# Kernel tuning notes

Hardware: AMD Instinct MI355X
Metric: run time of the kernel (lower is better)

The kernel has to match this reference:

```python
import jax, jax.numpy as jnp
import numpy as np

B, S, H, DK = 8, 2048, 1024, 64


def setup_inputs() -> dict:
    key = jax.random.key(0)
    ks = jax.random.split(key, 8)
    x = jax.random.normal(ks[0], (B, S, H), dtype=jnp.float32)
    # padding at the tail: positions >= length are pad (True)
    lengths = jax.random.randint(ks[1], (B,), S // 2, S + 1)
    padding_mask = jnp.arange(S)[None, :] >= lengths[:, None]  # [B,S] bool, True = pad
    sc = 1.0 / np.sqrt(H)
    Wq = jax.random.normal(ks[2], (H, DK), dtype=jnp.float32) * sc
    Wk = jax.random.normal(ks[3], (H, DK), dtype=jnp.float32) * sc
    Wv = jax.random.normal(ks[4], (H, DK), dtype=jnp.float32) * sc
    bq = jnp.zeros((DK,), dtype=jnp.float32)
    bk = jnp.zeros((DK,), dtype=jnp.float32)
    bv = jnp.zeros((DK,), dtype=jnp.float32)
    return {"x": x, "padding_mask": padding_mask, "Wq": Wq, "bq": bq,
            "Wk": Wk, "bk": bk, "Wv": Wv, "bv": bv}


def reference(x, padding_mask, Wq, bq, Wk, bk, Wv, bv):
    # Single-head attention, dropout_pe = 0 (identity), masking=True (causal).
    d_k = Wq.shape[-1]
    Q = jnp.einsum('bsh,hd->bsd', x, Wq) + bq
    K = jnp.einsum('bsh,hd->bsd', x, Wk) + bk
    V = jnp.einsum('bsh,hd->bsd', x, Wv) + bv
    scores = jnp.einsum('bqd,bkd->bqk', Q, K) / jnp.sqrt(jnp.asarray(d_k, x.dtype))
    neg_inf = jnp.finfo(scores.dtype).min
    # padding mask over keys: [B,1,S]
    scores = jnp.where(padding_mask[:, None, :], neg_inf, scores)
    # causal mask: strictly upper triangular is disallowed
    seq = scores.shape[-1]
    causal = jnp.triu(jnp.ones((seq, seq), dtype=bool), k=1)
    scores = jnp.where(causal[None, :, :], neg_inf, scores)
    W = jax.nn.softmax(scores, axis=-1)
    # zero out attention rows for padded query positions: [B,S,1]
    W = jnp.where(padding_mask[:, :, None], 0.0, W)
    return jnp.einsum('bqk,bkd->bqd', W, V)
```

## Files before the change

kernel.cpp:

```cpp
#include <hip/hip_runtime.h>
#include <hip/hip_bf16.h>

#define NB 8
#define SEQ 2048
#define HD 1024
#define DK 64

#define QSCALE 0.1803368801111244f
#define FIXMAX2 11.541560327111708f

typedef __attribute__((ext_vector_type(4))) float f32x4;
typedef __attribute__((ext_vector_type(8))) short bf16x8;
typedef __attribute__((ext_vector_type(4))) unsigned short u16x4;

__device__ __forceinline__ short f2bf(float f) {
    union { float f; unsigned u; } v; v.f = f;
    unsigned r = v.u + 0x7fffu + ((v.u >> 16) & 1u);
    return (short)(r >> 16);
}
__device__ __forceinline__ bf16x8 pack8(f32x4 v0, f32x4 v1) {
    union { bf16x8 v; __hip_bfloat162 h[4]; } u;
    u.h[0] = __float22bfloat162_rn(make_float2(v0[0], v0[1]));
    u.h[1] = __float22bfloat162_rn(make_float2(v0[2], v0[3]));
    u.h[2] = __float22bfloat162_rn(make_float2(v1[0], v1[1]));
    u.h[3] = __float22bfloat162_rn(make_float2(v1[2], v1[3]));
    return u.v;
}

__global__ void prep_kernel(const unsigned* __restrict__ mask,
                            const float* __restrict__ Wq, const float* __restrict__ Wk,
                            const float* __restrict__ Wv,
                            int* __restrict__ lengths, short* __restrict__ Wp) {
    if (blockIdx.x < 768) {
        int idx = blockIdx.x * 256 + threadIdx.x;
        int j = idx & 7, lane = (idx >> 3) & 63;
        int slot = idx >> 9;
        int fr = slot % 3, q2 = slot / 3;
        int kh = q2 & 1, cg = (q2 >> 1) & 3, kbg = q2 >> 3;
        int g = lane >> 4, c = lane & 15;
        int n = cg * 3 + fr;
        int m = n >> 2, colm = (n & 3) * 16 + c;
        int k = kbg * 64 + kh * 32 + g * 8 + j;
        const float* W = (m == 0) ? Wq : (m == 1) ? Wk : Wv;
        Wp[idx] = f2bf(W[(size_t)k * DK + colm]);
        return;
    }
    __shared__ int sdet;
    __shared__ int scnt;
    int b = blockIdx.x - 768, t = threadIdx.x;
    if (t == 0) { sdet = 0; scnt = 0; }
    __syncthreads();
    int det = 0;
    for (int i = t; i < 4096; i += 256) {
        unsigned w = mask[i];
        if (w > 1u && w != 0x3F800000u) det = 1;
    }
    if (det) atomicOr(&sdet, 1);
    __syncthreads();
    int cnt = 0;
    if (sdet) {
        const unsigned char* m8 = (const unsigned char*)mask;
        for (int s = t; s < SEQ; s += 256) cnt += (m8[b * SEQ + s] == 0) ? 1 : 0;
    } else {
        for (int s = t; s < SEQ; s += 256) cnt += (mask[b * SEQ + s] == 0u) ? 1 : 0;
    }
    atomicAdd(&scnt, cnt);
    __syncthreads();
    if (t == 0) lengths[b] = scnt;
}

__global__ __launch_bounds__(512, 2) void qkv_kernel(
    const float* __restrict__ x,
    const float* __restrict__ bq, const float* __restrict__ bk, const float* __restrict__ bv,
    const short* __restrict__ Wp,
    short* __restrict__ Q, short* __restrict__ K, short* __restrict__ Vt) {
    __shared__ float xs[2][64][64];
    int t = threadIdx.x;
    int w = t >> 6, lane = t & 63;
    int g = lane >> 4, c = lane & 15;
    int rg = w >> 2, cg = w & 3;
    int r0 = blockIdx.x * 64;
    int bb = r0 >> 11, sbase = r0 & (SEQ - 1);

    int srow = t >> 3, sc8 = t & 7;
    const float* xsrc = x + (size_t)(r0 + srow) * HD + sc8 * 8;
    float* wbase = &xs[0][0][0];
    int wo0 = srow * 64 + (((2 * sc8) ^ (srow & 15)) << 2);
    int wo1 = srow * 64 + (((2 * sc8 + 1) ^ (srow & 15)) << 2);

    const short* wpw = Wp + (size_t)cg * 2 * 3 * 512 + (size_t)lane * 8;

    f32x4 z = {0.f, 0.f, 0.f, 0.f};
    f32x4 acc[2][3];
    #pragma unroll
    for (int rf = 0; rf < 2; rf++)
        #pragma unroll
        for (int fr = 0; fr < 3; fr++) acc[rf][fr] = z;

    {
        f32x4 x0 = *(const f32x4*)xsrc;
        f32x4 x1 = *(const f32x4*)(xsrc + 4);
        *(f32x4*)(wbase + wo0) = x0;
        *(f32x4*)(wbase + wo1) = x1;
    }
    bf16x8 Bc[2][3];
    #pragma unroll
    for (int kh = 0; kh < 2; kh++)
        #pragma unroll
        for (int fr = 0; fr < 3; fr++)
            Bc[kh][fr] = *(const bf16x8*)(wpw + kh * 1536 + fr * 512);
    __syncthreads();

    const float* rbase0 = &xs[0][0][0] + (rg * 32 + c) * 64;
    #pragma unroll
    for (int kbg = 0; kbg < 16; kbg++) {
        int cur = kbg & 1;
        f32x4 nx0, nx1;
        bf16x8 Bn[2][3];
        if (kbg < 15) {
            const float* p = xsrc + (kbg + 1) * 64;
            nx0 = *(const f32x4*)p;
            nx1 = *(const f32x4*)(p + 4);
            #pragma unroll
            for (int kh = 0; kh < 2; kh++)
                #pragma unroll
                for (int fr = 0; fr < 3; fr++)
                    Bn[kh][fr] = *(const bf16x8*)(wpw + (kbg + 1) * 12288 + kh * 1536 + fr * 512);
        }
        bf16x8 Af[2][2];
        #pragma unroll
        for (int rf = 0; rf < 2; rf++)
            #pragma unroll
            for (int kh = 0; kh < 2; kh++) {
                const float* rp = rbase0 + cur * 4096 + rf * 1024;
                int lg = kh * 8 + 2 * g;
                f32x4 lo = *(const f32x4*)(rp + ((lg ^ c) << 2));
                f32x4 hi = *(const f32x4*)(rp + (((lg + 1) ^ c) << 2));
                Af[rf][kh] = pack8(lo, hi);
            }
        #pragma unroll
        for (int kh = 0; kh < 2; kh++)
            #pragma unroll
            for (int fr = 0; fr < 3; fr++)
                #pragma unroll
                for (int rf = 0; rf < 2; rf++)
                    acc[rf][fr] = __builtin_amdgcn_mfma_f32_16x16x32_bf16(Af[rf][kh], Bc[kh][fr], acc[rf][fr], 0, 0, 0);
        if (kbg < 15) {
            float* wb = wbase + (cur ^ 1) * 4096;
            *(f32x4*)(wb + wo0) = nx0;
            *(f32x4*)(wb + wo1) = nx1;
            #pragma unroll
            for (int kh = 0; kh < 2; kh++)
                #pragma unroll
                for (int fr = 0; fr < 3; fr++) Bc[kh][fr] = Bn[kh][fr];
        }
        __syncthreads();
    }

    #pragma unroll
    for (int rf = 0; rf < 2; rf++)
        #pragma unroll
        for (int fr = 0; fr < 3; fr++) {
            int n = cg * 3 + fr;
            int m = n >> 2, colm = (n & 3) * 16 + c;
            const float* bias = (m == 0) ? bq : (m == 1) ? bk : bv;
            float bv_ = bias[colm];
            if (m == 2) {
                u16x4 pk;
                #pragma unroll
                for (int j = 0; j < 4; j++) pk[j] = (unsigned short)f2bf(acc[rf][fr][j] + bv_);
                int srw = sbase + rg * 32 + rf * 16 + 4 * g;
                *(u16x4*)(Vt + (size_t)bb * DK * SEQ + (size_t)colm * SEQ + srw) = pk;
            } else {
                #pragma unroll
                for (int j = 0; j < 4; j++) {
                    int row = r0 + rg * 32 + rf * 16 + 4 * g + j;
                    float s = acc[rf][fr][j] + bv_;
                    if (m == 0) Q[(size_t)row * DK + colm] = f2bf(s * QSCALE);
                    else        K[(size_t)row * DK + colm] = f2bf(s);
                }
            }
        }
}

__global__ __launch_bounds__(256) void attn_kernel(
    const short* __restrict__ Q, const short* __restrict__ K_, const short* __restrict__ Vt,
    const int* __restrict__ lengths, float* __restrict__ out) {
    __shared__ float macc[4][32][66];
    __shared__ float ll[4][32];
    short* plds = (short*)&macc[0][0][0];

    int bid = blockIdx.x;
    int qt = 63 - (bid & 63);
    int b = bid >> 6;
    int len = lengths[b];
    int qbase = qt * 32;
    int t = threadIdx.x;
    int w = t >> 6, lane = t & 63;
    int g = lane >> 4, c = lane & 15;

    if (qbase >= len) {
        int row = t >> 3, seg = t & 7;
        float* op = out + ((size_t)b * SEQ + qbase + row) * DK + seg * 8;
        #pragma unroll
        for (int i = 0; i < 8; i++) op[i] = 0.f;
        return;
    }

    int kend = min(len, qbase + 32);
    int ntiles = (kend + 63) >> 6;
    const short* Qb = Q + ((size_t)b * SEQ + qbase) * DK;
    const short* Kb = K_ + (size_t)b * SEQ * DK;
    const short* Vb = Vt + (size_t)b * DK * SEQ;

    bf16x8 qa[2][2];
    #pragma unroll
    for (int f = 0; f < 2; f++)
        #pragma unroll
        for (int kh = 0; kh < 2; kh++)
            qa[f][kh] = *(const bf16x8*)(Qb + (f * 16 + c) * DK + kh * 32 + g * 8);

    int rowcap[2][4];
    #pragma unroll
    for (int f = 0; f < 2; f++)
        #pragma unroll
        for (int j = 0; j < 4; j++)
            rowcap[f][j] = min(qbase + f * 16 + 4 * g + j, len - 1);

    f32x4 z = {0.f, 0.f, 0.f, 0.f};
    f32x4 acc[2][4];
    float l_r[2][4];
    #pragma unroll
    for (int f = 0; f < 2; f++) {
        #pragma unroll
        for (int n = 0; n < 4; n++) acc[f][n] = z;
        #pragma unroll
        for (int j = 0; j < 4; j++) l_r[f][j] = 0.f;
    }

    short* pldsw = plds + w * 2240;

    bf16x8 kh0[2][2];
    if (w < ntiles) {
        #pragma unroll
        for (int kt = 0; kt < 2; kt++) {
            const short* kp = Kb + (size_t)(w * 64 + kt * 16 + c) * DK + g * 8;
            kh0[kt][0] = *(const bf16x8*)kp;
            kh0[kt][1] = *(const bf16x8*)(kp + 32);
        }
    }

    for (int tt = w; tt < ntiles; tt += 4) {
        int kb = tt * 64;
        bf16x8 kh1[2][2];
        #pragma unroll
        for (int kt = 0; kt < 2; kt++) {
            const short* kp = Kb + (size_t)(kb + 32 + kt * 16 + c) * DK + g * 8;
            kh1[kt][0] = *(const bf16x8*)kp;
            kh1[kt][1] = *(const bf16x8*)(kp + 32);
        }
        f32x4 sf[2][4];
        #pragma unroll
        for (int kt = 0; kt < 2; kt++)
            #pragma unroll
            for (int f = 0; f < 2; f++) {
                f32x4 t0 = __builtin_amdgcn_mfma_f32_16x16x32_bf16(qa[f][0], kh0[kt][0], z, 0, 0, 0);
                sf[f][kt] = __builtin_amdgcn_mfma_f32_16x16x32_bf16(qa[f][1], kh0[kt][1], t0, 0, 0, 0);
            }
        if (tt + 4 < ntiles) {
            #pragma unroll
            for (int kt = 0; kt < 2; kt++) {
                const short* kp = Kb + (size_t)((tt + 4) * 64 + kt * 16 + c) * DK + g * 8;
                kh0[kt][0] = *(const bf16x8*)kp;
                kh0[kt][1] = *(const bf16x8*)(kp + 32);
            }
        }
        bf16x8 vr[4][2];
        #pragma unroll
        for (int n = 0; n < 4; n++) {
            const short* vp = Vb + (size_t)(n * 16 + c) * SEQ + kb + g * 8;
            vr[n][0] = *(const bf16x8*)vp;
            vr[n][1] = *(const bf16x8*)(vp + 32);
        }
        #pragma unroll
        for (int kt = 0; kt < 2; kt++)
            #pragma unroll
            for (int f = 0; f < 2; f++) {
                f32x4 t0 = __builtin_amdgcn_mfma_f32_16x16x32_bf16(qa[f][0], kh1[kt][0], z, 0, 0, 0);
                sf[f][kt + 2] = __builtin_amdgcn_mfma_f32_16x16x32_bf16(qa[f][1], kh1[kt][1], t0, 0, 0, 0);
            }
        #pragma unroll
        for (int kt = 0; kt < 4; kt++) {
            int key = kb + kt * 16 + c;
            #pragma unroll
            for (int f = 0; f < 2; f++)
                #pragma unroll
                for (int j = 0; j < 4; j++) {
                    float s = (key > rowcap[f][j]) ? -1e30f : sf[f][kt][j];
                    float p = exp2f(s - FIXMAX2);
                    sf[f][kt][j] = p;
                    l_r[f][j] += p;
                }
        }
        #pragma unroll
        for (int f = 0; f < 2; f++)
            #pragma unroll
            for (int kt = 0; kt < 4; kt++)
                #pragma unroll
                for (int j = 0; j < 4; j++)
                    pldsw[f * 1120 + (4 * g + j) * 70 + kt * 16 + c] = f2bf(sf[f][kt][j]);
        #pragma unroll
        for (int f = 0; f < 2; f++) {
            bf16x8 pa0 = *(const bf16x8*)(pldsw + f * 1120 + c * 70 + g * 8);
            bf16x8 pa1 = *(const bf16x8*)(pldsw + f * 1120 + c * 70 + 32 + g * 8);
            #pragma unroll
            for (int n = 0; n < 4; n++) {
                acc[f][n] = __builtin_amdgcn_mfma_f32_16x16x32_bf16(pa0, vr[n][0], acc[f][n], 0, 0, 0);
                acc[f][n] = __builtin_amdgcn_mfma_f32_16x16x32_bf16(pa1, vr[n][1], acc[f][n], 0, 0, 0);
            }
        }
    }

    #pragma unroll
    for (int d = 1; d < 16; d <<= 1)
        #pragma unroll
        for (int f = 0; f < 2; f++)
            #pragma unroll
            for (int j = 0; j < 4; j++) l_r[f][j] += __shfl_xor(l_r[f][j], d);

    __syncthreads();
    #pragma unroll
    for (int f = 0; f < 2; f++)
        #pragma unroll
        for (int n = 0; n < 4; n++)
            #pragma unroll
            for (int j = 0; j < 4; j++)
                macc[w][f * 16 + 4 * g + j][n * 16 + c] = acc[f][n][j];
    if (c == 0) {
        #pragma unroll
        for (int f = 0; f < 2; f++)
            #pragma unroll
            for (int j = 0; j < 4; j++)
                ll[w][f * 16 + 4 * g + j] = l_r[f][j];
    }
    __syncthreads();
    {
        int row = t >> 3, seg = t & 7;
        int r = qbase + row;
        float* op = out + ((size_t)b * SEQ + r) * DK + seg * 8;
        float o[8];
        #pragma unroll
        for (int i = 0; i < 8; i++) o[i] = 0.f;
        if (r < len) {
            float L = ll[0][row] + ll[1][row] + ll[2][row] + ll[3][row];
            #pragma unroll
            for (int wv = 0; wv < 4; wv++)
                #pragma unroll
                for (int i = 0; i < 8; i++) o[i] += macc[wv][row][seg * 8 + i];
            float inv = 1.f / L;
            #pragma unroll
            for (int i = 0; i < 8; i++) o[i] *= inv;
        }
        #pragma unroll
        for (int i = 0; i < 8; i++) op[i] = o[i];
    }
}

extern "C" void kernel_launch(void* const* d_in, const int* in_sizes, int n_in,
                              void* d_out, int out_size, void* d_ws, size_t ws_size,
                              hipStream_t stream) {
    const float* x  = (const float*)d_in[0];
    const unsigned* mask = (const unsigned*)d_in[1];
    const float* Wq = (const float*)d_in[2];
    const float* bq = (const float*)d_in[3];
    const float* Wk = (const float*)d_in[4];
    const float* bk = (const float*)d_in[5];
    const float* Wv = (const float*)d_in[6];
    const float* bv = (const float*)d_in[7];
    float* out = (float*)d_out;

    char* ws = (char*)d_ws;
    int*   lengths = (int*)ws;
    short* Wp = (short*)(ws + 256);
    short* Q  = (short*)(ws + 393472);
    short* K  = (short*)(ws + 2490624);
    short* Vt = (short*)(ws + 4587776);

    hipLaunchKernelGGL(prep_kernel, dim3(776), dim3(256), 0, stream, mask, Wq, Wk, Wv, lengths, Wp);
    hipLaunchKernelGGL(qkv_kernel, dim3(256), dim3(512), 0, stream,
                       x, bq, bk, bv, Wp, Q, K, Vt);
    hipLaunchKernelGGL(attn_kernel, dim3(NB * 64), dim3(256), 0, stream,
                       Q, K, Vt, lengths, out);
}
```

Before: 63.65 us.

## Halve QKV row tile and use 8 waves per attention block

The QKV projection kernel now handles 32 rows per block with 256 threads, so it launches twice as many blocks to fill more CUs. The attention kernel moves to 512 threads (8 waves), each wave taking every eighth key tile, with LDS reduction buffers grown to match. The hand-written K register prefetch across iterations is removed in favor of loading the whole 64-key tile at once. Epilogue and zero-fill store mappings are adjusted for the new thread count. The risks are more LDS per attention block, a larger cross-wave reduction, and exposed K-load latency now that the explicit prefetch is gone.

After: 69.50 us. +9.2%, slower.

```diff
diff --git a/kernel.cpp b/kernel.cpp
--- a/kernel.cpp
+++ b/kernel.cpp
@@ -69,17 +69,16 @@
     if (t == 0) lengths[b] = scnt;
 }
 
-__global__ __launch_bounds__(512, 2) void qkv_kernel(
+__global__ __launch_bounds__(256, 2) void qkv_kernel(
     const float* __restrict__ x,
     const float* __restrict__ bq, const float* __restrict__ bk, const float* __restrict__ bv,
     const short* __restrict__ Wp,
     short* __restrict__ Q, short* __restrict__ K, short* __restrict__ Vt) {
-    __shared__ float xs[2][64][64];
+    __shared__ float xs[2][32][64];
     int t = threadIdx.x;
-    int w = t >> 6, lane = t & 63;
+    int cg = t >> 6, lane = t & 63;
     int g = lane >> 4, c = lane & 15;
-    int rg = w >> 2, cg = w & 3;
-    int r0 = blockIdx.x * 64;
+    int r0 = blockIdx.x * 32;
     int bb = r0 >> 11, sbase = r0 & (SEQ - 1);
 
     int srow = t >> 3, sc8 = t & 7;
@@ -88,7 +87,7 @@
     int wo0 = srow * 64 + (((2 * sc8) ^ (srow & 15)) << 2);
     int wo1 = srow * 64 + (((2 * sc8 + 1) ^ (srow & 15)) << 2);
 
-    const short* wpw = Wp + (size_t)cg * 2 * 3 * 512 + (size_t)lane * 8;
+    const short* wpw = Wp + (size_t)cg * 3072 + (size_t)lane * 8;
 
     f32x4 z = {0.f, 0.f, 0.f, 0.f};
     f32x4 acc[2][3];
@@ -111,7 +110,7 @@
             Bc[kh][fr] = *(const bf16x8*)(wpw + kh * 1536 + fr * 512);
     __syncthreads();
 
-    const float* rbase0 = &xs[0][0][0] + (rg * 32 + c) * 64;
+    const float* rbase0 = &xs[0][0][0] + c * 64;
     #pragma unroll
     for (int kbg = 0; kbg < 16; kbg++) {
         int cur = kbg & 1;
@@ -132,7 +131,7 @@
         for (int rf = 0; rf < 2; rf++)
             #pragma unroll
             for (int kh = 0; kh < 2; kh++) {
-                const float* rp = rbase0 + cur * 4096 + rf * 1024;
+                const float* rp = rbase0 + cur * 2048 + rf * 1024;
                 int lg = kh * 8 + 2 * g;
                 f32x4 lo = *(const f32x4*)(rp + ((lg ^ c) << 2));
                 f32x4 hi = *(const f32x4*)(rp + (((lg + 1) ^ c) << 2));
@@ -146,7 +145,7 @@
                 for (int rf = 0; rf < 2; rf++)
                     acc[rf][fr] = __builtin_amdgcn_mfma_f32_16x16x32_bf16(Af[rf][kh], Bc[kh][fr], acc[rf][fr], 0, 0, 0);
         if (kbg < 15) {
-            float* wb = wbase + (cur ^ 1) * 4096;
+            float* wb = wbase + (cur ^ 1) * 2048;
             *(f32x4*)(wb + wo0) = nx0;
             *(f32x4*)(wb + wo1) = nx1;
             #pragma unroll
@@ -169,12 +168,12 @@
                 u16x4 pk;
                 #pragma unroll
                 for (int j = 0; j < 4; j++) pk[j] = (unsigned short)f2bf(acc[rf][fr][j] + bv_);
-                int srw = sbase + rg * 32 + rf * 16 + 4 * g;
+                int srw = sbase + rf * 16 + 4 * g;
                 *(u16x4*)(Vt + (size_t)bb * DK * SEQ + (size_t)colm * SEQ + srw) = pk;
             } else {
                 #pragma unroll
                 for (int j = 0; j < 4; j++) {
-                    int row = r0 + rg * 32 + rf * 16 + 4 * g + j;
+                    int row = r0 + rf * 16 + 4 * g + j;
                     float s = acc[rf][fr][j] + bv_;
                     if (m == 0) Q[(size_t)row * DK + colm] = f2bf(s * QSCALE);
                     else        K[(size_t)row * DK + colm] = f2bf(s);
@@ -183,11 +182,11 @@
         }
 }
 
-__global__ __launch_bounds__(256) void attn_kernel(
+__global__ __launch_bounds__(512, 4) void attn_kernel(
     const short* __restrict__ Q, const short* __restrict__ K_, const short* __restrict__ Vt,
     const int* __restrict__ lengths, float* __restrict__ out) {
-    __shared__ float macc[4][32][66];
-    __shared__ float ll[4][32];
+    __shared__ float macc[8][32][66];
+    __shared__ float ll[8][32];
     short* plds = (short*)&macc[0][0][0];
 
     int bid = blockIdx.x;
@@ -200,10 +199,10 @@
     int g = lane >> 4, c = lane & 15;
 
     if (qbase >= len) {
-        int row = t >> 3, seg = t & 7;
-        float* op = out + ((size_t)b * SEQ + qbase + row) * DK + seg * 8;
-        #pragma unroll
-        for (int i = 0; i < 8; i++) op[i] = 0.f;
+        int row = t >> 4, col0 = (t & 15) * 4;
+        float* op = out + ((size_t)b * SEQ + qbase + row) * DK + col0;
+        f32x4 zz = {0.f, 0.f, 0.f, 0.f};
+        *(f32x4*)op = zz;
         return;
     }
 
@@ -240,41 +239,23 @@
 
     short* pldsw = plds + w * 2240;
 
-    bf16x8 kh0[2][2];
-    if (w < ntiles) {
-        #pragma unroll
-        for (int kt = 0; kt < 2; kt++) {
-            const short* kp = Kb + (size_t)(w * 64 + kt * 16 + c) * DK + g * 8;
-            kh0[kt][0] = *(const bf16x8*)kp;
-            kh0[kt][1] = *(const bf16x8*)(kp + 32);
-        }
-    }
-
-    for (int tt = w; tt < ntiles; tt += 4) {
+    for (int tt = w; tt < ntiles; tt += 8) {
         int kb = tt * 64;
-        bf16x8 kh1[2][2];
-        #pragma unroll
-        for (int kt = 0; kt < 2; kt++) {
-            const short* kp = Kb + (size_t)(kb + 32 + kt * 16 + c) * DK + g * 8;
-            kh1[kt][0] = *(const bf16x8*)kp;
-            kh1[kt][1] = *(const bf16x8*)(kp + 32);
+        bf16x8 kr[4][2];
+        #pragma unroll
+        for (int kt = 0; kt < 4; kt++) {
+            const short* kp = Kb + (size_t)(kb + kt * 16 + c) * DK + g * 8;
+            kr[kt][0] = *(const bf16x8*)kp;
+            kr[kt][1] = *(const bf16x8*)(kp + 32);
         }
         f32x4 sf[2][4];
         #pragma unroll
-        for (int kt = 0; kt < 2; kt++)
+        for (int kt = 0; kt < 4; kt++)
             #pragma unroll
             for (int f = 0; f < 2; f++) {
-                f32x4 t0 = __builtin_amdgcn_mfma_f32_16x16x32_bf16(qa[f][0], kh0[kt][0], z, 0, 0, 0);
-                sf[f][kt] = __builtin_amdgcn_mfma_f32_16x16x32_bf16(qa[f][1], kh0[kt][1], t0, 0, 0, 0);
+                f32x4 t0 = __builtin_amdgcn_mfma_f32_16x16x32_bf16(qa[f][0], kr[kt][0], z, 0, 0, 0);
+                sf[f][kt] = __builtin_amdgcn_mfma_f32_16x16x32_bf16(qa[f][1], kr[kt][1], t0, 0, 0, 0);
             }
-        if (tt + 4 < ntiles) {
-            #pragma unroll
-            for (int kt = 0; kt < 2; kt++) {
-                const short* kp = Kb + (size_t)((tt + 4) * 64 + kt * 16 + c) * DK + g * 8;
-                kh0[kt][0] = *(const bf16x8*)kp;
-                kh0[kt][1] = *(const bf16x8*)(kp + 32);
-            }
-        }
         bf16x8 vr[4][2];
         #pragma unroll
         for (int n = 0; n < 4; n++) {
@@ -282,13 +263,6 @@
             vr[n][0] = *(const bf16x8*)vp;
             vr[n][1] = *(const bf16x8*)(vp + 32);
         }
-        #pragma unroll
-        for (int kt = 0; kt < 2; kt++)
-            #pragma unroll
-            for (int f = 0; f < 2; f++) {
-                f32x4 t0 = __builtin_amdgcn_mfma_f32_16x16x32_bf16(qa[f][0], kh1[kt][0], z, 0, 0, 0);
-                sf[f][kt + 2] = __builtin_amdgcn_mfma_f32_16x16x32_bf16(qa[f][1], kh1[kt][1], t0, 0, 0, 0);
-            }
         #pragma unroll
         for (int kt = 0; kt < 4; kt++) {
             int key = kb + kt * 16 + c;
@@ -345,24 +319,24 @@
     }
     __syncthreads();
     {
-        int row = t >> 3, seg = t & 7;
+        int row = t >> 4, seg = t & 15;
         int r = qbase + row;
-        float* op = out + ((size_t)b * SEQ + r) * DK + seg * 8;
-        float o[8];
-        #pragma unroll
-        for (int i = 0; i < 8; i++) o[i] = 0.f;
+        float* op = out + ((size_t)b * SEQ + r) * DK + seg * 4;
+        float o[4] = {0.f, 0.f, 0.f, 0.f};
         if (r < len) {
-            float L = ll[0][row] + ll[1][row] + ll[2][row] + ll[3][row];
-            #pragma unroll
-            for (int wv = 0; wv < 4; wv++)
-                #pragma unroll
-                for (int i = 0; i < 8; i++) o[i] += macc[wv][row][seg * 8 + i];
+            float L = 0.f;
+            #pragma unroll
+            for (int wv = 0; wv < 8; wv++) L += ll[wv][row];
+            #pragma unroll
+            for (int wv = 0; wv < 8; wv++)
+                #pragma unroll
+                for (int i = 0; i < 4; i++) o[i] += macc[wv][row][seg * 4 + i];
             float inv = 1.f / L;
             #pragma unroll
-            for (int i = 0; i < 8; i++) o[i] *= inv;
-        }
-        #pragma unroll
-        for (int i = 0; i < 8; i++) op[i] = o[i];
+            for (int i = 0; i < 4; i++) o[i] *= inv;
+        }
+        #pragma unroll
+        for (int i = 0; i < 4; i++) op[i] = o[i];
     }
 }
 
@@ -387,8 +361,8 @@
     short* Vt = (short*)(ws + 4587776);
 
     hipLaunchKernelGGL(prep_kernel, dim3(776), dim3(256), 0, stream, mask, Wq, Wk, Wv, lengths, Wp);
-    hipLaunchKernelGGL(qkv_kernel, dim3(256), dim3(512), 0, stream,
+    hipLaunchKernelGGL(qkv_kernel, dim3(512), dim3(256), 0, stream,
                        x, bq, bk, bv, Wp, Q, K, Vt);
-    hipLaunchKernelGGL(attn_kernel, dim3(NB * 64), dim3(256), 0, stream,
+    hipLaunchKernelGGL(attn_kernel, dim3(NB * 64), dim3(512), 0, stream,
                        Q, K, Vt, lengths, out);
 }
```
